# Kernel optimization log

Hardware: AMD Instinct MI355X
Metric: run time of the kernel (lower is better)

## Reference

```python
import jax, jax.numpy as jnp
import numpy as np

D_MODEL = 1024
N_HEADS = 16
D_HEAD = D_MODEL // N_HEADS
LN_EPS = 1e-5


def setup_inputs() -> dict:
    key = jax.random.key(0)
    ks = jax.random.split(key, 10)
    B, N = 2, 2048
    s = 1.0 / np.sqrt(D_MODEL)
    return {
        "x": jax.random.normal(ks[0], (B, N, D_MODEL), dtype=jnp.float32),
        "Wq": jax.random.normal(ks[1], (D_MODEL, D_MODEL), dtype=jnp.float32) * s,
        "bq": jnp.zeros((D_MODEL,), dtype=jnp.float32),
        "Wk": jax.random.normal(ks[2], (D_MODEL, D_MODEL), dtype=jnp.float32) * s,
        "bk": jnp.zeros((D_MODEL,), dtype=jnp.float32),
        "Wv": jax.random.normal(ks[3], (D_MODEL, D_MODEL), dtype=jnp.float32) * s,
        "bv": jnp.zeros((D_MODEL,), dtype=jnp.float32),
        "Wo": jax.random.normal(ks[4], (D_MODEL, D_MODEL), dtype=jnp.float32) * s,
        "bo": jnp.zeros((D_MODEL,), dtype=jnp.float32),
        "ln_gamma": jnp.ones((D_MODEL,), dtype=jnp.float32),
        "ln_beta": jnp.zeros((D_MODEL,), dtype=jnp.float32),
    }


def reference(x, Wq, bq, Wk, bk, Wv, bv, Wo, bo, ln_gamma, ln_beta):
    B, N, _ = x.shape
    # QKV projections -> [B, H, N, dh]
    def proj(W, b):
        return (x @ W.T + b).reshape(B, N, N_HEADS, D_HEAD).transpose(0, 2, 1, 3)
    Q, K, V = proj(Wq, bq), proj(Wk, bk), proj(Wv, bv)
    # scaled scores [B, H, N, N] with causal mask (is_mask=True)
    scores = jnp.einsum("bhqd,bhkd->bhqk", Q, K) / np.sqrt(D_HEAD)
    causal = jnp.tril(jnp.ones((N, N), dtype=bool))
    scores = jnp.where(causal, scores, -jnp.inf)
    attn = jax.nn.softmax(scores, axis=-1)  # dropout p=0 (eval)
    ctx = jnp.einsum("bhqk,bhkd->bhqd", attn, V)  # [B, H, N, dh]
    ctx = ctx.transpose(0, 2, 1, 3).reshape(B, N, D_MODEL)
    out = ctx @ Wo.T + bo + x  # output proj + residual
    # LayerNorm over last dim
    mu = out.mean(-1, keepdims=True)
    var = out.var(-1, keepdims=True)
    return (out - mu) / jnp.sqrt(var + LN_EPS) * ln_gamma + ln_beta
```

## Files before the change

### kernel.cpp

```cpp
#include <hip/hip_runtime.h>
#include <type_traits>

#define D_MODEL 1024
#define NHEADS 16
#define DHEAD 64
#define SEQ 2048
#define BATCH 2
#define MROWS (BATCH*SEQ)
#define NQT (SEQ/64)

typedef unsigned short ushort_t;
typedef unsigned int   u32;
using bf16x8 = __attribute__((ext_vector_type(8))) __bf16;
using bf16x4 = __attribute__((ext_vector_type(4))) __bf16;
using us4    = __attribute__((ext_vector_type(4))) unsigned short;
using us8    = __attribute__((ext_vector_type(8))) unsigned short;
using f32x4  = __attribute__((ext_vector_type(4))) float;
using f32x2  = __attribute__((ext_vector_type(2))) float;

#define QSCALE 0.18033688011112042f

__device__ __forceinline__ float fast_exp2(float x) {
#if __has_builtin(__builtin_amdgcn_exp2f)
    return __builtin_amdgcn_exp2f(x);
#else
    return __expf(x * 0.6931471805599453f);
#endif
}

__device__ __forceinline__ void gl2lds(const ushort_t* g, ushort_t* l) {
    __builtin_amdgcn_global_load_lds(
        (const __attribute__((address_space(1))) unsigned int*)g,
        (__attribute__((address_space(3))) unsigned int*)l,
        16, 0, 0);
}

__global__ __launch_bounds__(256) void cvt_kernel(
    const float* __restrict__ x,
    const float* __restrict__ wq, const float* __restrict__ wk,
    const float* __restrict__ wv, const float* __restrict__ wo,
    ushort_t* __restrict__ xb,
    ushort_t* __restrict__ wqb, ushort_t* __restrict__ wkb,
    ushort_t* __restrict__ wvb, ushort_t* __restrict__ wob)
{
    const size_t XN = (size_t)MROWS * D_MODEL;
    const size_t WN = (size_t)D_MODEL * D_MODEL;
    size_t i = ((size_t)blockIdx.x * 256 + threadIdx.x) * 4;
    const float* s; ushort_t* d; size_t off;
    if (i < XN) { s = x; d = xb; off = i; }
    else {
        size_t j = i - XN;
        int w = (int)(j / WN);
        off = j - (size_t)w * WN;
        s = (w == 0) ? wq : (w == 1) ? wk : (w == 2) ? wv : wo;
        d = (w == 0) ? wqb : (w == 1) ? wkb : (w == 2) ? wvb : wob;
    }
    const f32x4 v = *(const f32x4*)(s + off);
    bf16x4 o;
    #pragma unroll
    for (int t = 0; t < 4; ++t) o[t] = (__bf16)v[t];
    *(bf16x4*)(d + off) = o;
}

template<typename OutT, bool RES>
__global__ __launch_bounds__(256, 3) void gemm_nt(
    const ushort_t* __restrict__ A,
    const ushort_t* __restrict__ W0, const ushort_t* __restrict__ W1, const ushort_t* __restrict__ W2,
    const float* __restrict__ b0, const float* __restrict__ b1, const float* __restrict__ b2,
    const float* __restrict__ res,
    OutT* __restrict__ Y0, OutT* __restrict__ Y1, OutT* __restrict__ Y2,
    float qsc)
{
    constexpr int K = D_MODEL;
    __shared__ ushort_t As[2][128 * 32];
    __shared__ ushort_t Ws[2][128 * 32];

    const int z = blockIdx.z;
    const ushort_t* W  = (z == 0) ? W0 : (z == 1) ? W1 : W2;
    const float* bias  = (z == 0) ? b0 : (z == 1) ? b1 : b2;
    OutT* Y            = (z == 0) ? Y0 : (z == 1) ? Y1 : Y2;
    const float sc     = (z == 0) ? qsc : 1.0f;

    const int i0 = blockIdx.x * 128;
    const int j0 = blockIdx.y * 128;
    const int tid  = threadIdx.x;
    const int lane = tid & 63;
    const int w    = tid >> 6;
    const int wm   = (w >> 1) * 64;
    const int wn   = (w & 1) * 64;
    const int l15  = lane & 15;
    const int quad = lane >> 4;

    const int srow = lane >> 2;
    const int scol = (lane & 3) * 8;
    const int c0 = w * 2, c1 = w * 2 + 1;
    const ushort_t* gA0 = A + (size_t)(i0 + c0 * 16 + srow) * K + scol;
    const ushort_t* gA1 = A + (size_t)(i0 + c1 * 16 + srow) * K + scol;
    const ushort_t* gW0 = W + (size_t)(j0 + c0 * 16 + srow) * K + scol;
    const ushort_t* gW1 = W + (size_t)(j0 + c1 * 16 + srow) * K + scol;

    f32x4 acc[4][4] = {};

    for (int k0 = 0; k0 < K; k0 += 64) {
        gl2lds(gA0 + k0,      &As[0][c0 * 512]);
        gl2lds(gA1 + k0,      &As[0][c1 * 512]);
        gl2lds(gA0 + k0 + 32, &As[1][c0 * 512]);
        gl2lds(gA1 + k0 + 32, &As[1][c1 * 512]);
        gl2lds(gW0 + k0,      &Ws[0][c0 * 512]);
        gl2lds(gW1 + k0,      &Ws[0][c1 * 512]);
        gl2lds(gW0 + k0 + 32, &Ws[1][c0 * 512]);
        gl2lds(gW1 + k0 + 32, &Ws[1][c1 * 512]);
        __syncthreads();

        #pragma unroll
        for (int s = 0; s < 2; ++s) {
            bf16x8 af[4], wf[4];
            #pragma unroll
            for (int m = 0; m < 4; ++m)
                af[m] = *(const bf16x8*)&As[s][(wm + m * 16 + l15) * 32 + quad * 8];
            #pragma unroll
            for (int n = 0; n < 4; ++n)
                wf[n] = *(const bf16x8*)&Ws[s][(wn + n * 16 + l15) * 32 + quad * 8];
            #pragma unroll
            for (int m = 0; m < 4; ++m)
                #pragma unroll
                for (int n = 0; n < 4; ++n)
                    acc[m][n] = __builtin_amdgcn_mfma_f32_16x16x32_bf16(wf[n], af[m], acc[m][n], 0, 0, 0);
        }
        __syncthreads();
    }

    #pragma unroll
    for (int n = 0; n < 4; ++n) {
        const int col = j0 + wn + n * 16 + quad * 4;
        const f32x4 bv = *(const f32x4*)&bias[col];
        #pragma unroll
        for (int m = 0; m < 4; ++m) {
            const int row = i0 + wm + m * 16 + l15;
            if constexpr (std::is_same<OutT, float>::value) {
                f32x4 v;
                #pragma unroll
                for (int r = 0; r < 4; ++r) v[r] = acc[m][n][r] + bv[r];
                if constexpr (RES) {
                    const f32x4 rv = *(const f32x4*)&res[(size_t)row * D_MODEL + col];
                    #pragma unroll
                    for (int r = 0; r < 4; ++r) v[r] += rv[r];
                }
                *(f32x4*)&Y[(size_t)row * D_MODEL + col] = v;
            } else {
                bf16x4 pk;
                #pragma unroll
                for (int r = 0; r < 4; ++r) pk[r] = (__bf16)((acc[m][n][r] + bv[r]) * sc);
                *(bf16x4*)&Y[(size_t)row * D_MODEL + col] = pk;
            }
        }
    }
}

#define KD 64

__global__ __launch_bounds__(256, 4) void attn_kernel(
    const ushort_t* __restrict__ Qg, const ushort_t* __restrict__ Kg,
    const ushort_t* __restrict__ Vg, ushort_t* __restrict__ Og,
    float* __restrict__ wso, float* __restrict__ wsml)
{
    __shared__ __align__(16) ushort_t Kt[2][64 * KD];
    __shared__ __align__(16) ushort_t Vt[2][64 * KD];
    __shared__ __align__(16) ushort_t Pw[64 * KD];

    const int bh = blockIdx.x;
    const int b = bh >> 4;
    const int h = bh & 15;

    const int y = blockIdx.y;
    int qt, kt0, kt1;
    bool heavy;
    if (y < 32) {
        qt = 16 + (y >> 1);
        const int nkt = qt + 1;
        const int hh = nkt >> 1;
        heavy = true;
        if (y & 1) { kt0 = hh; kt1 = nkt; }
        else       { kt0 = 0;  kt1 = hh;  }
    } else {
        qt = 47 - y;
        kt0 = 0; kt1 = qt + 1; heavy = false;
    }
    const int part = y & 1;
    const int q0 = qt * 64;

    const int tid  = threadIdx.x;
    const int lane = tid & 63;
    const int w    = tid >> 6;
    const int l15  = lane & 15;
    const int quad = lane >> 4;

    const size_t headoff = (size_t)h * DHEAD;
    const ushort_t* Kbase = Kg + (size_t)(b * SEQ) * D_MODEL + headoff;
    const ushort_t* Vbase = Vg + (size_t)(b * SEQ) * D_MODEL + headoff;

    const int krow = tid >> 3;
    const int kb   = tid & 7;
    const int vkey = tid & 63;
    const int dc0  = tid >> 6;
    const int dc1  = dc0 + 4;

    const int rx = (l15 & 7) << 3;
    const int cs0 = (quad * 8) ^ rx;
    const int cs1 = (32 + quad * 8) ^ rx;
    int pwc[4];
    #pragma unroll
    for (int f = 0; f < 4; ++f) pwc[f] = (f * 16 + quad * 4) ^ rx;
    ushort_t* PwRow = &Pw[(w * 16 + l15) * KD];

    const int kwa = krow * KD + ((kb * 8) ^ ((krow & 7) << 3));

    const int qg = q0 + w * 16 + l15;
    const size_t qrow = (size_t)(b * SEQ + qg) * D_MODEL + headoff;
    const bf16x8 qf0 = *(const bf16x8*)&Qg[qrow + quad * 8];
    const bf16x8 qf1 = *(const bf16x8*)&Qg[qrow + 32 + quad * 8];

    bf16x8 onesf;
    #pragma unroll
    for (int j = 0; j < 8; ++j) onesf[j] = (__bf16)1.0f;

    float m_run = -1e30f;
    f32x4 o[4] = {};
    f32x4 o4 = {};

    us8 kp0, kp1, vp0, vp1;
    const size_t koff0 = (size_t)(kt0 * 64) * D_MODEL;
    kp0 = *(const us8*)&Kbase[koff0 + (size_t)krow * D_MODEL + kb * 8];
    kp1 = *(const us8*)&Kbase[koff0 + (size_t)(32 + krow) * D_MODEL + kb * 8];
    vp0 = *(const us8*)&Vbase[koff0 + (size_t)vkey * D_MODEL + dc0 * 8];
    vp1 = *(const us8*)&Vbase[koff0 + (size_t)vkey * D_MODEL + dc1 * 8];
    *(us8*)&Kt[0][kwa]           = kp0;
    *(us8*)&Kt[0][kwa + 32 * KD] = kp1;
    #pragma unroll
    for (int j = 0; j < 8; ++j) {
        Vt[0][(dc0 * 8 + j) * KD + (vkey ^ (j << 3))] = vp0[j];
        Vt[0][(dc1 * 8 + j) * KD + (vkey ^ (j << 3))] = vp1[j];
    }
    __syncthreads();

    for (int kt = kt0; kt < kt1; ++kt) {
        const int cur = (kt - kt0) & 1;
        const int nxt = cur ^ 1;
        const bool pre = (kt + 1 < kt1);
        if (pre) {
            const size_t koff = (size_t)((kt + 1) * 64) * D_MODEL;
            kp0 = *(const us8*)&Kbase[koff + (size_t)krow * D_MODEL + kb * 8];
            kp1 = *(const us8*)&Kbase[koff + (size_t)(32 + krow) * D_MODEL + kb * 8];
            vp0 = *(const us8*)&Vbase[koff + (size_t)vkey * D_MODEL + dc0 * 8];
            vp1 = *(const us8*)&Vbase[koff + (size_t)vkey * D_MODEL + dc1 * 8];
        }

        f32x4 sv[4];
        __builtin_amdgcn_s_setprio(1);
        #pragma unroll
        for (int f = 0; f < 4; ++f) {
            const int rbase = (f * 16 + l15) * KD;
            const bf16x8 kf0 = *(const bf16x8*)&Kt[cur][rbase + cs0];
            const bf16x8 kf1 = *(const bf16x8*)&Kt[cur][rbase + cs1];
            f32x4 s = {};
            s = __builtin_amdgcn_mfma_f32_16x16x32_bf16(kf0, qf0, s, 0, 0, 0);
            s = __builtin_amdgcn_mfma_f32_16x16x32_bf16(kf1, qf1, s, 0, 0, 0);
            sv[f] = s;
        }
        __builtin_amdgcn_s_setprio(0);

        if (kt == qt) {
            #pragma unroll
            for (int f = 0; f < 4; ++f)
                #pragma unroll
                for (int r = 0; r < 4; ++r) {
                    const int kg = kt * 64 + f * 16 + quad * 4 + r;
                    sv[f][r] = (kg <= qg) ? sv[f][r] : -1e30f;
                }
        }

        float mf[4];
        #pragma unroll
        for (int f = 0; f < 4; ++f)
            mf[f] = fmaxf(fmaxf(sv[f][0], sv[f][1]), fmaxf(sv[f][2], sv[f][3]));
        float mx = fmaxf(fmaxf(mf[0], mf[1]), fmaxf(mf[2], mf[3]));
        mx = fmaxf(mx, __shfl_xor(mx, 16));
        mx = fmaxf(mx, __shfl_xor(mx, 32));

        if (!__all(mx <= m_run + 8.0f)) {
            const float mn = fmaxf(m_run, mx);
            const float al = fast_exp2(m_run - mn);
            m_run = mn;
            #pragma unroll
            for (int t = 0; t < 4; ++t)
                #pragma unroll
                for (int r = 0; r < 4; ++r) o[t][r] *= al;
            o4[0] *= al;
        }

        #pragma unroll
        for (int f = 0; f < 4; ++f) {
            bf16x4 pk;
            #pragma unroll
            for (int r = 0; r < 4; ++r)
                pk[r] = (__bf16)fast_exp2(sv[f][r] - m_run);
            *(bf16x4*)&PwRow[pwc[f]] = pk;
        }
        __asm__ volatile("s_waitcnt lgkmcnt(0)" ::: "memory");

        __builtin_amdgcn_s_setprio(1);
        #pragma unroll
        for (int s = 0; s < 2; ++s) {
            const bf16x8 pf = *(const bf16x8*)&PwRow[s ? cs1 : cs0];
            #pragma unroll
            for (int t = 0; t < 4; ++t) {
                const bf16x8 vf = *(const bf16x8*)&Vt[cur][(t * 16 + l15) * KD + (s ? cs1 : cs0)];
                o[t] = __builtin_amdgcn_mfma_f32_16x16x32_bf16(vf, pf, o[t], 0, 0, 0);
            }
            o4 = __builtin_amdgcn_mfma_f32_16x16x32_bf16(onesf, pf, o4, 0, 0, 0);
        }
        __builtin_amdgcn_s_setprio(0);

        if (pre) {
            *(us8*)&Kt[nxt][kwa]           = kp0;
            *(us8*)&Kt[nxt][kwa + 32 * KD] = kp1;
            #pragma unroll
            for (int j = 0; j < 8; ++j) {
                Vt[nxt][(dc0 * 8 + j) * KD + (vkey ^ (j << 3))] = vp0[j];
                Vt[nxt][(dc1 * 8 + j) * KD + (vkey ^ (j << 3))] = vp1[j];
            }
        }
        __asm__ volatile("s_waitcnt lgkmcnt(0)\n\ts_barrier" ::: "memory");
    }

    if (!heavy) {
        const float inv = 1.f / o4[0];
        const size_t orow = (size_t)(b * SEQ + qg) * D_MODEL + headoff;
        #pragma unroll
        for (int t = 0; t < 4; ++t) {
            bf16x4 pk;
            #pragma unroll
            for (int r = 0; r < 4; ++r) pk[r] = (__bf16)(o[t][r] * inv);
            *(bf16x4*)&Og[orow + t * 16 + quad * 4] = pk;
        }
    } else {
        const int T = (bh * 16 + (qt - 16)) * 2 + part;
        float* wo = wso + (size_t)T * 4096 + (size_t)(w * 16 + l15) * 64;
        #pragma unroll
        for (int t = 0; t < 4; ++t)
            *(f32x4*)&wo[t * 16 + quad * 4] = o[t];
        if (quad == 0) {
            f32x2 ml = { m_run, o4[0] };
            *(f32x2*)&wsml[(size_t)(T * 64 + w * 16 + l15) * 2] = ml;
        }
    }
}

__global__ __launch_bounds__(256) void attn_combine(
    const float* __restrict__ wso, const float* __restrict__ wsml,
    ushort_t* __restrict__ Og)
{
    const int gid = blockIdx.x * 256 + threadIdx.x;
    const int row = gid >> 4;
    const int dp  = (gid & 15) * 4;
    const int bh  = row >> 10;
    const int rr  = row & 1023;
    const int qh  = rr >> 6;
    const int q   = rr & 63;
    const int T0  = (bh * 16 + qh) * 2;

    const f32x2 ml0 = *(const f32x2*)&wsml[(size_t)(T0 * 64 + q) * 2];
    const f32x2 ml1 = *(const f32x2*)&wsml[(size_t)((T0 + 1) * 64 + q) * 2];
    const float M  = fmaxf(ml0[0], ml1[0]);
    const float a0 = fast_exp2(ml0[0] - M);
    const float a1 = fast_exp2(ml1[0] - M);
    const float inv = 1.0f / (ml0[1] * a0 + ml1[1] * a1);

    const f32x4 o0 = *(const f32x4*)&wso[(size_t)T0 * 4096 + q * 64 + dp];
    const f32x4 o1 = *(const f32x4*)&wso[(size_t)(T0 + 1) * 4096 + q * 64 + dp];

    const int b = bh >> 4;
    const int h = bh & 15;
    const int qg = (16 + qh) * 64 + q;
    bf16x4 pk;
    #pragma unroll
    for (int r = 0; r < 4; ++r)
        pk[r] = (__bf16)((o0[r] * a0 + o1[r] * a1) * inv);
    *(bf16x4*)&Og[(size_t)(b * SEQ + qg) * D_MODEL + h * DHEAD + dp] = pk;
}

__global__ __launch_bounds__(256) void ln_kernel(
    const float* __restrict__ X, const float* __restrict__ g,
    const float* __restrict__ bta, float* __restrict__ out)
{
    __shared__ float r1[4], r2[4];
    const int row = blockIdx.x;
    const int tid = threadIdx.x;
    const float* p = X + (size_t)row * D_MODEL;
    float v[4]; float s1 = 0.f, s2 = 0.f;
    #pragma unroll
    for (int i = 0; i < 4; ++i) { v[i] = p[tid + 256 * i]; s1 += v[i]; s2 += v[i] * v[i]; }
    #pragma unroll
    for (int d = 32; d >= 1; d >>= 1) { s1 += __shfl_xor(s1, d); s2 += __shfl_xor(s2, d); }
    if ((tid & 63) == 0) { r1[tid >> 6] = s1; r2[tid >> 6] = s2; }
    __syncthreads();
    s1 = r1[0] + r1[1] + r1[2] + r1[3];
    s2 = r2[0] + r2[1] + r2[2] + r2[3];
    const float mu  = s1 * (1.f / D_MODEL);
    const float var = s2 * (1.f / D_MODEL) - mu * mu;
    const float rstd = rsqrtf(var + 1e-5f);
    #pragma unroll
    for (int i = 0; i < 4; ++i) {
        const int c = tid + 256 * i;
        out[(size_t)row * D_MODEL + c] = (v[i] - mu) * rstd * g[c] + bta[c];
    }
}

extern "C" void kernel_launch(void* const* d_in, const int* in_sizes, int n_in,
                              void* d_out, int out_size, void* d_ws, size_t ws_size,
                              hipStream_t stream) {
    const float* x     = (const float*)d_in[0];
    const float* Wq    = (const float*)d_in[1];
    const float* bq    = (const float*)d_in[2];
    const float* Wk    = (const float*)d_in[3];
    const float* bk    = (const float*)d_in[4];
    const float* Wv    = (const float*)d_in[5];
    const float* bv    = (const float*)d_in[6];
    const float* Wo    = (const float*)d_in[7];
    const float* bo    = (const float*)d_in[8];
    const float* gamma = (const float*)d_in[9];
    const float* beta  = (const float*)d_in[10];

    const size_t XN = (size_t)MROWS * D_MODEL;
    const size_t WN = (size_t)D_MODEL * D_MODEL;
    ushort_t* wsp = (ushort_t*)d_ws;
    ushort_t* xb  = wsp;
    ushort_t* Yq  = wsp + XN;
    ushort_t* Yk  = wsp + 2 * XN;
    ushort_t* Yv  = wsp + 3 * XN;
    ushort_t* Wqb = wsp + 4 * XN;
    ushort_t* Wkb = Wqb + WN;
    ushort_t* Wvb = Wkb + WN;
    ushort_t* Wob = Wvb + WN;
    ushort_t* ctx = xb;
    float*    pre = (float*)d_out;

    float* wso  = (float*)(wsp + 4 * XN + 4 * WN);
    float* wsml = wso + (size_t)1024 * 4096;

    cvt_kernel<<<dim3(8192), 256, 0, stream>>>(x, Wq, Wk, Wv, Wo, xb, Wqb, Wkb, Wvb, Wob);

    gemm_nt<ushort_t, false><<<dim3(MROWS / 128, D_MODEL / 128, 3), 256, 0, stream>>>(
        xb, Wqb, Wkb, Wvb, bq, bk, bv, nullptr, Yq, Yk, Yv, QSCALE);

    attn_kernel<<<dim3(BATCH * NHEADS, 48), 256, 0, stream>>>(Yq, Yk, Yv, ctx, wso, wsml);

    attn_combine<<<dim3(2048), 256, 0, stream>>>(wso, wsml, ctx);

    gemm_nt<float, true><<<dim3(MROWS / 128, D_MODEL / 128, 1), 256, 0, stream>>>(
        ctx, Wob, Wob, Wob, bo, bo, bo, x, pre, pre, pre, 1.0f);

    ln_kernel<<<dim3(MROWS), 256, 0, stream>>>(pre, gamma, beta, (float*)d_out);
}
```

Measured before the change: 204.9 us.

## Process two 64-row query tiles per attention block to reuse K/V tiles

Each attention workgroup now handles 128 query rows (two 64-row tiles) instead of 64, so every K/V tile staged in LDS feeds twice as many MFMAs. This halves the global K/V traffic and LDS staging per query row. The grid shrinks from 48 to 24 tiles per head, and the split-K work for heavy tiles and the combine kernel are re-indexed to match. The cost is more registers (occupancy hint lowered from 4 to 3), a larger P buffer in LDS, and fewer blocks in flight.

```diff
diff --git a/kernel.cpp b/kernel.cpp
--- a/kernel.cpp
+++ b/kernel.cpp
@@ -159,35 +159,39 @@
 
 #define KD 64
 
-__global__ __launch_bounds__(256, 4) void attn_kernel(
+__global__ __launch_bounds__(256, 3) void attn_kernel(
     const ushort_t* __restrict__ Qg, const ushort_t* __restrict__ Kg,
     const ushort_t* __restrict__ Vg, ushort_t* __restrict__ Og,
     float* __restrict__ wso, float* __restrict__ wsml)
 {
     __shared__ __align__(16) ushort_t Kt[2][64 * KD];
     __shared__ __align__(16) ushort_t Vt[2][64 * KD];
-    __shared__ __align__(16) ushort_t Pw[64 * KD];
+    __shared__ __align__(16) ushort_t Pw[128 * KD];
 
     const int bh = blockIdx.x;
     const int b = bh >> 4;
     const int h = bh & 15;
 
     const int y = blockIdx.y;
-    int qt, kt0, kt1;
+    int qp, kt0, kt1, part;
     bool heavy;
-    if (y < 32) {
-        qt = 16 + (y >> 1);
-        const int nkt = qt + 1;
-        const int hh = nkt >> 1;
+    if (y < 16) {
+        qp = 15 - (y >> 1);
+        part = y & 1;
+        const int nkt = 2 * qp + 2;
+        const int hh = qp + 1;
         heavy = true;
-        if (y & 1) { kt0 = hh; kt1 = nkt; }
-        else       { kt0 = 0;  kt1 = hh;  }
+        if (part) { kt0 = hh; kt1 = nkt; }
+        else      { kt0 = 0;  kt1 = hh;  }
     } else {
-        qt = 47 - y;
-        kt0 = 0; kt1 = qt + 1; heavy = false;
-    }
-    const int part = y & 1;
-    const int q0 = qt * 64;
+        qp = 23 - y;
+        part = 0;
+        kt0 = 0; kt1 = 2 * qp + 2;
+        heavy = false;
+    }
+    const int qtL = 2 * qp;
+    const int qtU = 2 * qp + 1;
+    const int q0 = qp * 128;
 
     const int tid  = threadIdx.x;
     const int lane = tid & 63;
@@ -211,22 +215,27 @@
     int pwc[4];
     #pragma unroll
     for (int f = 0; f < 4; ++f) pwc[f] = (f * 16 + quad * 4) ^ rx;
-    ushort_t* PwRow = &Pw[(w * 16 + l15) * KD];
+    ushort_t* PwRowL = &Pw[(w * 16 + l15) * KD];
+    ushort_t* PwRowU = &Pw[(64 + w * 16 + l15) * KD];
 
     const int kwa = krow * KD + ((kb * 8) ^ ((krow & 7) << 3));
 
-    const int qg = q0 + w * 16 + l15;
-    const size_t qrow = (size_t)(b * SEQ + qg) * D_MODEL + headoff;
-    const bf16x8 qf0 = *(const bf16x8*)&Qg[qrow + quad * 8];
-    const bf16x8 qf1 = *(const bf16x8*)&Qg[qrow + 32 + quad * 8];
+    const int qgL = q0 + w * 16 + l15;
+    const int qgU = q0 + 64 + w * 16 + l15;
+    const size_t qrowL = (size_t)(b * SEQ + qgL) * D_MODEL + headoff;
+    const size_t qrowU = (size_t)(b * SEQ + qgU) * D_MODEL + headoff;
+    const bf16x8 qf0L = *(const bf16x8*)&Qg[qrowL + quad * 8];
+    const bf16x8 qf1L = *(const bf16x8*)&Qg[qrowL + 32 + quad * 8];
+    const bf16x8 qf0U = *(const bf16x8*)&Qg[qrowU + quad * 8];
+    const bf16x8 qf1U = *(const bf16x8*)&Qg[qrowU + 32 + quad * 8];
 
     bf16x8 onesf;
     #pragma unroll
     for (int j = 0; j < 8; ++j) onesf[j] = (__bf16)1.0f;
 
-    float m_run = -1e30f;
-    f32x4 o[4] = {};
-    f32x4 o4 = {};
+    float m_runL = -1e30f, m_runU = -1e30f;
+    f32x4 oL[4] = {}, oU[4] = {};
+    f32x4 o4L = {}, o4U = {};
 
     us8 kp0, kp1, vp0, vp1;
     const size_t koff0 = (size_t)(kt0 * 64) * D_MODEL;
@@ -247,6 +256,7 @@
         const int cur = (kt - kt0) & 1;
         const int nxt = cur ^ 1;
         const bool pre = (kt + 1 < kt1);
+        const bool actL = (kt <= qtL);
         if (pre) {
             const size_t koff = (size_t)((kt + 1) * 64) * D_MODEL;
             kp0 = *(const us8*)&Kbase[koff + (size_t)krow * D_MODEL + kb * 8];
@@ -255,69 +265,122 @@
             vp1 = *(const us8*)&Vbase[koff + (size_t)vkey * D_MODEL + dc1 * 8];
         }
 
-        f32x4 sv[4];
+        f32x4 svL[4], svU[4];
         __builtin_amdgcn_s_setprio(1);
         #pragma unroll
         for (int f = 0; f < 4; ++f) {
             const int rbase = (f * 16 + l15) * KD;
             const bf16x8 kf0 = *(const bf16x8*)&Kt[cur][rbase + cs0];
             const bf16x8 kf1 = *(const bf16x8*)&Kt[cur][rbase + cs1];
-            f32x4 s = {};
-            s = __builtin_amdgcn_mfma_f32_16x16x32_bf16(kf0, qf0, s, 0, 0, 0);
-            s = __builtin_amdgcn_mfma_f32_16x16x32_bf16(kf1, qf1, s, 0, 0, 0);
-            sv[f] = s;
+            f32x4 sU = {};
+            sU = __builtin_amdgcn_mfma_f32_16x16x32_bf16(kf0, qf0U, sU, 0, 0, 0);
+            sU = __builtin_amdgcn_mfma_f32_16x16x32_bf16(kf1, qf1U, sU, 0, 0, 0);
+            svU[f] = sU;
+            f32x4 sL = {};
+            sL = __builtin_amdgcn_mfma_f32_16x16x32_bf16(kf0, qf0L, sL, 0, 0, 0);
+            sL = __builtin_amdgcn_mfma_f32_16x16x32_bf16(kf1, qf1L, sL, 0, 0, 0);
+            svL[f] = sL;
         }
         __builtin_amdgcn_s_setprio(0);
 
-        if (kt == qt) {
+        if (kt == qtU) {
             #pragma unroll
             for (int f = 0; f < 4; ++f)
                 #pragma unroll
                 for (int r = 0; r < 4; ++r) {
                     const int kg = kt * 64 + f * 16 + quad * 4 + r;
-                    sv[f][r] = (kg <= qg) ? sv[f][r] : -1e30f;
+                    svU[f][r] = (kg <= qgU) ? svU[f][r] : -1e30f;
                 }
         }
-
-        float mf[4];
-        #pragma unroll
-        for (int f = 0; f < 4; ++f)
-            mf[f] = fmaxf(fmaxf(sv[f][0], sv[f][1]), fmaxf(sv[f][2], sv[f][3]));
-        float mx = fmaxf(fmaxf(mf[0], mf[1]), fmaxf(mf[2], mf[3]));
-        mx = fmaxf(mx, __shfl_xor(mx, 16));
-        mx = fmaxf(mx, __shfl_xor(mx, 32));
-
-        if (!__all(mx <= m_run + 8.0f)) {
-            const float mn = fmaxf(m_run, mx);
-            const float al = fast_exp2(m_run - mn);
-            m_run = mn;
-            #pragma unroll
-            for (int t = 0; t < 4; ++t)
-                #pragma unroll
-                for (int r = 0; r < 4; ++r) o[t][r] *= al;
-            o4[0] *= al;
-        }
-
-        #pragma unroll
-        for (int f = 0; f < 4; ++f) {
-            bf16x4 pk;
-            #pragma unroll
-            for (int r = 0; r < 4; ++r)
-                pk[r] = (__bf16)fast_exp2(sv[f][r] - m_run);
-            *(bf16x4*)&PwRow[pwc[f]] = pk;
+        if (kt == qtL) {
+            #pragma unroll
+            for (int f = 0; f < 4; ++f)
+                #pragma unroll
+                for (int r = 0; r < 4; ++r) {
+                    const int kg = kt * 64 + f * 16 + quad * 4 + r;
+                    svL[f][r] = (kg <= qgL) ? svL[f][r] : -1e30f;
+                }
+        }
+
+        {
+            float mf[4];
+            #pragma unroll
+            for (int f = 0; f < 4; ++f)
+                mf[f] = fmaxf(fmaxf(svU[f][0], svU[f][1]), fmaxf(svU[f][2], svU[f][3]));
+            float mx = fmaxf(fmaxf(mf[0], mf[1]), fmaxf(mf[2], mf[3]));
+            mx = fmaxf(mx, __shfl_xor(mx, 16));
+            mx = fmaxf(mx, __shfl_xor(mx, 32));
+            if (!__all(mx <= m_runU + 8.0f)) {
+                const float mn = fmaxf(m_runU, mx);
+                const float al = fast_exp2(m_runU - mn);
+                m_runU = mn;
+                #pragma unroll
+                for (int t = 0; t < 4; ++t)
+                    #pragma unroll
+                    for (int r = 0; r < 4; ++r) oU[t][r] *= al;
+                o4U[0] *= al;
+            }
+            #pragma unroll
+            for (int f = 0; f < 4; ++f) {
+                bf16x4 pk;
+                #pragma unroll
+                for (int r = 0; r < 4; ++r)
+                    pk[r] = (__bf16)fast_exp2(svU[f][r] - m_runU);
+                *(bf16x4*)&PwRowU[pwc[f]] = pk;
+            }
+        }
+        if (actL) {
+            float mf[4];
+            #pragma unroll
+            for (int f = 0; f < 4; ++f)
+                mf[f] = fmaxf(fmaxf(svL[f][0], svL[f][1]), fmaxf(svL[f][2], svL[f][3]));
+            float mx = fmaxf(fmaxf(mf[0], mf[1]), fmaxf(mf[2], mf[3]));
+            mx = fmaxf(mx, __shfl_xor(mx, 16));
+            mx = fmaxf(mx, __shfl_xor(mx, 32));
+            if (!__all(mx <= m_runL + 8.0f)) {
+                const float mn = fmaxf(m_runL, mx);
+                const float al = fast_exp2(m_runL - mn);
+                m_runL = mn;
+                #pragma unroll
+                for (int t = 0; t < 4; ++t)
+                    #pragma unroll
+                    for (int r = 0; r < 4; ++r) oL[t][r] *= al;
+                o4L[0] *= al;
+            }
+            #pragma unroll
+            for (int f = 0; f < 4; ++f) {
+                bf16x4 pk;
+                #pragma unroll
+                for (int r = 0; r < 4; ++r)
+                    pk[r] = (__bf16)fast_exp2(svL[f][r] - m_runL);
+                *(bf16x4*)&PwRowL[pwc[f]] = pk;
+            }
         }
         __asm__ volatile("s_waitcnt lgkmcnt(0)" ::: "memory");
 
         __builtin_amdgcn_s_setprio(1);
         #pragma unroll
         for (int s = 0; s < 2; ++s) {
-            const bf16x8 pf = *(const bf16x8*)&PwRow[s ? cs1 : cs0];
-            #pragma unroll
-            for (int t = 0; t < 4; ++t) {
-                const bf16x8 vf = *(const bf16x8*)&Vt[cur][(t * 16 + l15) * KD + (s ? cs1 : cs0)];
-                o[t] = __builtin_amdgcn_mfma_f32_16x16x32_bf16(vf, pf, o[t], 0, 0, 0);
-            }
-            o4 = __builtin_amdgcn_mfma_f32_16x16x32_bf16(onesf, pf, o4, 0, 0, 0);
+            const int cc = s ? cs1 : cs0;
+            const bf16x8 pfU = *(const bf16x8*)&PwRowU[cc];
+            if (actL) {
+                const bf16x8 pfL = *(const bf16x8*)&PwRowL[cc];
+                #pragma unroll
+                for (int t = 0; t < 4; ++t) {
+                    const bf16x8 vf = *(const bf16x8*)&Vt[cur][(t * 16 + l15) * KD + cc];
+                    oU[t] = __builtin_amdgcn_mfma_f32_16x16x32_bf16(vf, pfU, oU[t], 0, 0, 0);
+                    oL[t] = __builtin_amdgcn_mfma_f32_16x16x32_bf16(vf, pfL, oL[t], 0, 0, 0);
+                }
+                o4U = __builtin_amdgcn_mfma_f32_16x16x32_bf16(onesf, pfU, o4U, 0, 0, 0);
+                o4L = __builtin_amdgcn_mfma_f32_16x16x32_bf16(onesf, pfL, o4L, 0, 0, 0);
+            } else {
+                #pragma unroll
+                for (int t = 0; t < 4; ++t) {
+                    const bf16x8 vf = *(const bf16x8*)&Vt[cur][(t * 16 + l15) * KD + cc];
+                    oU[t] = __builtin_amdgcn_mfma_f32_16x16x32_bf16(vf, pfU, oU[t], 0, 0, 0);
+                }
+                o4U = __builtin_amdgcn_mfma_f32_16x16x32_bf16(onesf, pfU, o4U, 0, 0, 0);
+            }
         }
         __builtin_amdgcn_s_setprio(0);
 
@@ -334,24 +397,36 @@
     }
 
     if (!heavy) {
-        const float inv = 1.f / o4[0];
-        const size_t orow = (size_t)(b * SEQ + qg) * D_MODEL + headoff;
+        const float invL = 1.f / o4L[0];
+        const float invU = 1.f / o4U[0];
+        const size_t orowL = (size_t)(b * SEQ + qgL) * D_MODEL + headoff;
+        const size_t orowU = (size_t)(b * SEQ + qgU) * D_MODEL + headoff;
         #pragma unroll
         for (int t = 0; t < 4; ++t) {
-            bf16x4 pk;
-            #pragma unroll
-            for (int r = 0; r < 4; ++r) pk[r] = (__bf16)(o[t][r] * inv);
-            *(bf16x4*)&Og[orow + t * 16 + quad * 4] = pk;
+            bf16x4 pkL, pkU;
+            #pragma unroll
+            for (int r = 0; r < 4; ++r) {
+                pkL[r] = (__bf16)(oL[t][r] * invL);
+                pkU[r] = (__bf16)(oU[t][r] * invU);
+            }
+            *(bf16x4*)&Og[orowL + t * 16 + quad * 4] = pkL;
+            *(bf16x4*)&Og[orowU + t * 16 + quad * 4] = pkU;
         }
     } else {
-        const int T = (bh * 16 + (qt - 16)) * 2 + part;
-        float* wo = wso + (size_t)T * 4096 + (size_t)(w * 16 + l15) * 64;
+        const int T = (bh * 8 + (qp - 8)) * 2 + part;
+        const int rL = w * 16 + l15;
+        const int rU = 64 + w * 16 + l15;
+        float* wo = wso + (size_t)T * 8192;
         #pragma unroll
-        for (int t = 0; t < 4; ++t)
-            *(f32x4*)&wo[t * 16 + quad * 4] = o[t];
+        for (int t = 0; t < 4; ++t) {
+            *(f32x4*)&wo[(size_t)rL * 64 + t * 16 + quad * 4] = oL[t];
+            *(f32x4*)&wo[(size_t)rU * 64 + t * 16 + quad * 4] = oU[t];
+        }
         if (quad == 0) {
-            f32x2 ml = { m_run, o4[0] };
-            *(f32x2*)&wsml[(size_t)(T * 64 + w * 16 + l15) * 2] = ml;
+            f32x2 mlL = { m_runL, o4L[0] };
+            f32x2 mlU = { m_runU, o4U[0] };
+            *(f32x2*)&wsml[(size_t)(T * 128 + rL) * 2] = mlL;
+            *(f32x2*)&wsml[(size_t)(T * 128 + rU) * 2] = mlU;
         }
     }
 }
@@ -365,23 +440,23 @@
     const int dp  = (gid & 15) * 4;
     const int bh  = row >> 10;
     const int rr  = row & 1023;
-    const int qh  = rr >> 6;
-    const int q   = rr & 63;
-    const int T0  = (bh * 16 + qh) * 2;
-
-    const f32x2 ml0 = *(const f32x2*)&wsml[(size_t)(T0 * 64 + q) * 2];
-    const f32x2 ml1 = *(const f32x2*)&wsml[(size_t)((T0 + 1) * 64 + q) * 2];
+    const int qph = rr >> 7;
+    const int q   = rr & 127;
+    const int T0  = (bh * 8 + qph) * 2;
+
+    const f32x2 ml0 = *(const f32x2*)&wsml[(size_t)(T0 * 128 + q) * 2];
+    const f32x2 ml1 = *(const f32x2*)&wsml[(size_t)((T0 + 1) * 128 + q) * 2];
     const float M  = fmaxf(ml0[0], ml1[0]);
     const float a0 = fast_exp2(ml0[0] - M);
     const float a1 = fast_exp2(ml1[0] - M);
     const float inv = 1.0f / (ml0[1] * a0 + ml1[1] * a1);
 
-    const f32x4 o0 = *(const f32x4*)&wso[(size_t)T0 * 4096 + q * 64 + dp];
-    const f32x4 o1 = *(const f32x4*)&wso[(size_t)(T0 + 1) * 4096 + q * 64 + dp];
+    const f32x4 o0 = *(const f32x4*)&wso[(size_t)T0 * 8192 + q * 64 + dp];
+    const f32x4 o1 = *(const f32x4*)&wso[(size_t)(T0 + 1) * 8192 + q * 64 + dp];
 
     const int b = bh >> 4;
     const int h = bh & 15;
-    const int qg = (16 + qh) * 64 + q;
+    const int qg = 1024 + rr;
     bf16x4 pk;
     #pragma unroll
     for (int r = 0; r < 4; ++r)
@@ -446,14 +521,14 @@
     float*    pre = (float*)d_out;
 
     float* wso  = (float*)(wsp + 4 * XN + 4 * WN);
-    float* wsml = wso + (size_t)1024 * 4096;
+    float* wsml = wso + (size_t)512 * 8192;
 
     cvt_kernel<<<dim3(8192), 256, 0, stream>>>(x, Wq, Wk, Wv, Wo, xb, Wqb, Wkb, Wvb, Wob);
 
     gemm_nt<ushort_t, false><<<dim3(MROWS / 128, D_MODEL / 128, 3), 256, 0, stream>>>(
         xb, Wqb, Wkb, Wvb, bq, bk, bv, nullptr, Yq, Yk, Yv, QSCALE);
 
-    attn_kernel<<<dim3(BATCH * NHEADS, 48), 256, 0, stream>>>(Yq, Yk, Yv, ctx, wso, wsml);
+    attn_kernel<<<dim3(BATCH * NHEADS, 24), 256, 0, stream>>>(Yq, Yk, Yv, ctx, wso, wsml);
 
     attn_combine<<<dim3(2048), 256, 0, stream>>>(wso, wsml, ctx);
 
```

Result: slower. 209.7 us (+2.4%).
